# Optimization experiments

Hardware: AMD Instinct MI355X
Metric: run time of the kernel (lower is better)

## Reference

```python
import jax, jax.numpy as jnp
import numpy as np

B, T_TXT, DUR_MAX = 32, 512, 8


def setup_inputs() -> dict:
    key = jax.random.key(0)
    k1, _ = jax.random.split(key)
    # durations are integer-valued frame counts stored as float (module does dur.float())
    dur = jax.random.randint(k1, (B, T_TXT), 0, DUR_MAX).astype(jnp.float32)
    dur_padding = jnp.zeros((B, T_TXT), dtype=jnp.int32)
    return {"dur": dur, "dur_padding": dur_padding}


def reference(dur, dur_padding):
    alpha = 1.0  # default duration rescale coefficient
    d = jnp.round(dur * alpha).astype(jnp.int32)          # (B, T_txt)
    d = d * (1 - dur_padding)
    dur_cumsum = jnp.cumsum(d, axis=1)                     # (B, T_txt)
    dur_cumsum_prev = jnp.concatenate(
        [jnp.zeros_like(dur_cumsum[:, :1]), dur_cumsum[:, :-1]], axis=1)
    # T_speech = max total duration; data-dependent width, resolved eagerly
    T_mel = int(np.asarray(dur_cumsum[:, -1].max()))
    pos_idx = jnp.arange(T_mel)[None, None, :]             # (1, 1, T_mel)
    token_idx = jnp.arange(1, d.shape[1] + 1, dtype=jnp.int32)[None, :, None]  # (1, T_txt, 1)
    token_mask = (pos_idx >= dur_cumsum_prev[:, :, None]) & (pos_idx < dur_cumsum[:, :, None])
    mel2token = jnp.sum(token_idx * token_mask.astype(jnp.int32), axis=1)  # (B, T_mel)
    return mel2token
```

## Files before the change

kernel.cpp:

```cpp
#include <hip/hip_runtime.h>
#include <hip/hip_bf16.h>


#define T_TXT 512
#define BATCH 32

__global__ __launch_bounds__(T_TXT) void LengthRegulator_8169027797081_kernel(
    const float* __restrict__ dur, const int* __restrict__ pad,
    int* __restrict__ out, int T_mel) {
    __shared__ int cum[T_TXT];
    const int b = blockIdx.x;
    const int t = threadIdx.x;

    float v = dur[b * T_TXT + t];
    int d = (int)rintf(v);
    d *= (1 - pad[b * T_TXT + t]);
    cum[t] = d;
    __syncthreads();

    #pragma unroll
    for (int off = 1; off < T_TXT; off <<= 1) {
        int add = (t >= off) ? cum[t - off] : 0;
        __syncthreads();
        cum[t] += add;
        __syncthreads();
    }

    const int total = cum[T_TXT - 1];

    for (int p = t; p < T_mel; p += T_TXT) {
        int val = 0;
        if (p < total) {
            int lo = 0, hi = T_TXT - 1;
            while (lo < hi) {
                int mid = (lo + hi) >> 1;
                if (cum[mid] > p) hi = mid; else lo = mid + 1;
            }
            val = lo + 1;
        }
        out[b * T_mel + p] = val;
    }
}

extern "C" void kernel_launch(void* const* d_in, const int* in_sizes, int n_in,
                              void* d_out, int out_size, void* d_ws, size_t ws_size,
                              hipStream_t stream) {
    const float* dur = (const float*)d_in[0];
    const int* pad = (const int*)d_in[1];
    int* out = (int*)d_out;
    const int T_mel = out_size / BATCH;
    LengthRegulator_8169027797081_kernel<<<BATCH, T_TXT, 0, stream>>>(dur, pad, out, T_mel);
}
```

Measured before the change: 9.727 us.

## Use wave-shuffle scan and scatter token indices instead of binary search

Replaces the shared-memory Hillis-Steele scan, which needs many block barriers, with a per-wavefront shuffle scan followed by a single barrier to combine the wave totals. Instead of each output position binary-searching the cumulative sums, each token thread writes its own index directly into its duration span, and the tail beyond the row total is zero-filled. This removes the barrier-heavy scan and the search loops. In exchange, the stores are less coalesced because each thread writes a short, variable-length run.

```diff
diff --git a/kernel.cpp b/kernel.cpp
--- a/kernel.cpp
+++ b/kernel.cpp
@@ -4,42 +4,45 @@
 
 #define T_TXT 512
 #define BATCH 32
+#define NWAVES (T_TXT / 64)
 
 __global__ __launch_bounds__(T_TXT) void LengthRegulator_8169027797081_kernel(
     const float* __restrict__ dur, const int* __restrict__ pad,
     int* __restrict__ out, int T_mel) {
-    __shared__ int cum[T_TXT];
     const int b = blockIdx.x;
     const int t = threadIdx.x;
+    const int lane = t & 63;
+    const int w = t >> 6;
 
-    float v = dur[b * T_TXT + t];
-    int d = (int)rintf(v);
+    int d = (int)rintf(dur[b * T_TXT + t]);
     d *= (1 - pad[b * T_TXT + t]);
-    cum[t] = d;
+
+    int x = d;
+    #pragma unroll
+    for (int off = 1; off < 64; off <<= 1) {
+        int y = __shfl_up(x, off, 64);
+        if (lane >= off) x += y;
+    }
+
+    __shared__ int wsum[NWAVES];
+    if (lane == 63) wsum[w] = x;
     __syncthreads();
 
+    int base = 0, total = 0;
     #pragma unroll
-    for (int off = 1; off < T_TXT; off <<= 1) {
-        int add = (t >= off) ? cum[t - off] : 0;
-        __syncthreads();
-        cum[t] += add;
-        __syncthreads();
+    for (int i = 0; i < NWAVES; ++i) {
+        int s = wsum[i];
+        if (i < w) base += s;
+        total += s;
     }
 
-    const int total = cum[T_TXT - 1];
+    const int cum = base + x;
+    const int cum_prev = cum - d;
+    int* __restrict__ row = out + b * T_mel;
 
-    for (int p = t; p < T_mel; p += T_TXT) {
-        int val = 0;
-        if (p < total) {
-            int lo = 0, hi = T_TXT - 1;
-            while (lo < hi) {
-                int mid = (lo + hi) >> 1;
-                if (cum[mid] > p) hi = mid; else lo = mid + 1;
-            }
-            val = lo + 1;
-        }
-        out[b * T_mel + p] = val;
-    }
+    for (int p = cum_prev; p < cum; ++p) row[p] = t + 1;
+
+    for (int p = total + t; p < T_mel; p += T_TXT) row[p] = 0;
 }
 
 extern "C" void kernel_launch(void* const* d_in, const int* in_sizes, int n_in,
```

New measurement: 9.752 us. Within noise of the previous version (+0.3%).
